# Optimization experiments

Hardware: AMD Instinct MI355X
Metric: run time of the kernel (lower is better)

The kernel has to match this reference:

```python
import jax, jax.numpy as jnp
import numpy as np

B, S, D, H, HD, K, FF, G, E = 2, 2048, 512, 8, 64, 31, 2048, 4, 2
EPS = 1e-6


def _layer_norm(x, scale, bias):
    m = jnp.mean(x, axis=-1, keepdims=True)
    v = jnp.var(x, axis=-1, keepdims=True)
    return (x - m) * jax.lax.rsqrt(v + EPS) * scale + bias


def _forward(x, group_ids, p):
    (ln1_s, ln1_b, ck, cb, ln2_s, ln2_b,
     wq, bq, wk, bk, wv, bv, wo, bo, w1, b1, w2, b2) = p
    # ---- conv sublayer: LN -> Conv1d(SAME) -> gelu -> residual ----
    r = x
    h = _layer_norm(x, ln1_s, ln1_b)
    h = jax.lax.conv_general_dilated(h, ck, (1,), 'SAME',
                                     dimension_numbers=('NWC', 'WIO', 'NWC')) + cb
    x = jax.nn.gelu(h) + r
    # ---- self-attention sublayer: LN -> MHA -> residual ----
    r = x
    h = _layer_norm(x, ln2_s, ln2_b)
    q = jnp.einsum('bsd,dhk->bshk', h, wq) + bq   # [B,S,H,HD]
    k = jnp.einsum('bsd,dhk->bshk', h, wk) + bk
    v = jnp.einsum('bsd,dhk->bshk', h, wv) + bv
    scale = jnp.asarray(1.0 / np.sqrt(HD), h.dtype)
    att = jax.nn.softmax(jnp.einsum('bqhk,bshk->bhqs', q, k) * scale, axis=-1)
    o = jnp.einsum('bhqs,bshk->bqhk', att, v)
    x = jnp.einsum('bqhk,hkd->bqd', o, wo) + bo + r
    # ---- MoE sublayer: group tokens -> per-group experts -> mean -> combine ----
    r = x
    xf = x.reshape(-1, D)            # [N, D]
    gid = group_ids.reshape(-1)      # [N]
    # Each token routed by group_id gets the mean over that group's E experts.
    hid = jax.nn.gelu(jnp.einsum('nd,gedf->genf', xf, w1) + b1[:, :, None, :])  # [G,E,N,FF]
    ye = jnp.einsum('genf,gefd->gend', hid, w2) + b2[:, :, None, :]             # [G,E,N,D]
    yg = ye.mean(axis=1)                                                        # [G,N,D]
    sel = yg[gid, jnp.arange(gid.shape[0])]                                     # [N,D] combine by group id
    return sel.reshape(B, S, D) + r


def setup_inputs() -> dict:
    key = jax.random.key(0)
    ks = jax.random.split(key, 12)
    std = 0.02
    f32 = jnp.float32
    return {
        'x': jax.random.normal(ks[0], (B, S, D), f32),
        'group_ids': jax.random.randint(ks[1], (B, S), 0, G, jnp.int32),
        'ln1_scale': jnp.ones((D,), f32), 'ln1_bias': jnp.zeros((D,), f32),
        'conv_kernel': jax.random.normal(ks[2], (K, D, D), f32) * std,
        'conv_bias': jnp.zeros((D,), f32),
        'ln2_scale': jnp.ones((D,), f32), 'ln2_bias': jnp.zeros((D,), f32),
        'wq': jax.random.normal(ks[3], (D, H, HD), f32) * std, 'bq': jnp.zeros((H, HD), f32),
        'wk': jax.random.normal(ks[4], (D, H, HD), f32) * std, 'bk': jnp.zeros((H, HD), f32),
        'wv': jax.random.normal(ks[5], (D, H, HD), f32) * std, 'bv': jnp.zeros((H, HD), f32),
        'wo': jax.random.normal(ks[6], (H, HD, D), f32) * std, 'bo': jnp.zeros((D,), f32),
        'w1': jax.random.normal(ks[7], (G, E, D, FF), f32) * std, 'b1': jnp.zeros((G, E, FF), f32),
        'w2': jax.random.normal(ks[8], (G, E, FF, D), f32) * std, 'b2': jnp.zeros((G, E, D), f32),
    }


def reference(x, group_ids, ln1_scale, ln1_bias, conv_kernel, conv_bias,
              ln2_scale, ln2_bias, wq, bq, wk, bk, wv, bv, wo, bo,
              w1, b1, w2, b2):
    p = (ln1_scale, ln1_bias, conv_kernel, conv_bias, ln2_scale, ln2_bias,
         wq, bq, wk, bk, wv, bv, wo, bo, w1, b1, w2, b2)
    return _forward(x, group_ids, p)
```

## Files before the change

kernel.cpp:

```cpp
#include <hip/hip_runtime.h>
#include <hip/hip_bf16.h>
#include <math.h>
#include <stdint.h>

namespace {

constexpr int B_ = 2, S_ = 2048, D_ = 512, H_ = 8, HD_ = 64, K_ = 31,
              FF_ = 2048, G_ = 4, E_ = 2;
constexpr int N_ = B_ * S_;
constexpr int SP_ = S_ + 30;
constexpr float EPS_ = 1e-6f;
constexpr int PADCAP_ = 4608;

typedef __bf16 bf16x8 __attribute__((ext_vector_type(8)));
typedef unsigned short u16x8 __attribute__((ext_vector_type(8)));
typedef unsigned short u16x4 __attribute__((ext_vector_type(4)));
typedef float f32x4 __attribute__((ext_vector_type(4)));

__device__ __forceinline__ uint16_t f2bf(float f) {
  union { float f; uint32_t u; } v; v.f = f;
  uint32_t r = v.u + 0x7FFFu + ((v.u >> 16) & 1u);
  return (uint16_t)(r >> 16);
}
__device__ __forceinline__ float bf2f(uint16_t u) {
  union { uint32_t u; float f; } v; v.u = (uint32_t)u << 16;
  return v.f;
}

__device__ __forceinline__ float gelu_f(float x) {
  const float c = 0.7978845608028654f;
  return 0.5f * x * (1.0f + tanhf(c * (x + 0.044715f * x * x * x)));
}

#define GLOAD_LDS16(gsrc, ldst)                                              \
  __builtin_amdgcn_global_load_lds(                                          \
      (const __attribute__((address_space(1))) void*)(gsrc),                 \
      (__attribute__((address_space(3))) void*)(ldst), 16, 0, 0)

#define VMCNT(n) asm volatile("s_waitcnt vmcnt(" #n ")" ::: "memory")
#define MEMBAR asm volatile("" ::: "memory")
#define BARRIER __builtin_amdgcn_s_barrier()
#define PRIO1 __builtin_amdgcn_s_setprio(1)
#define PRIO0 __builtin_amdgcn_s_setprio(0)

__device__ __forceinline__ void kstep_swz(const char* As, const char* Bs,
                                          int wr, int wc, int l15, int g,
                                          f32x4 acc[4][4]) {
#pragma unroll
  for (int ks = 0; ks < 2; ++ks) {
    int co = (((ks << 2) | g) ^ (l15 & 7)) << 4;
    bf16x8 a[4], b[4];
#pragma unroll
    for (int m = 0; m < 4; ++m)
      a[m] = *(const bf16x8*)(As + (wr * 64 + m * 16 + l15) * 128 + co);
#pragma unroll
    for (int n = 0; n < 4; ++n)
      b[n] = *(const bf16x8*)(Bs + (wc * 64 + n * 16 + l15) * 128 + co);
    PRIO1;
#pragma unroll
    for (int m = 0; m < 4; ++m)
#pragma unroll
      for (int n = 0; n < 4; ++n)
        acc[m][n] = __builtin_amdgcn_mfma_f32_16x16x32_bf16(a[m], b[n], acc[m][n], 0, 0, 0);
    PRIO0;
  }
}

template <int NK>
__device__ __forceinline__ void gemm_k_dbuf64(const uint16_t* Ab, int lda,
                                              const uint16_t* Bb, int ldb,
                                              int t, int wr, int wc, int l15, int g,
                                              uint16_t (*As)[8192], uint16_t (*Bs)[8192],
                                              f32x4 acc[4][4]) {
  int r8 = t >> 3, clog = (t & 7) ^ (r8 & 7);
  int ubase = (t & ~63) * 8;
  auto stage = [&](int k0, int buf) {
#pragma unroll
    for (int pi = 0; pi < 4; ++pi) {
      int row = pi * 32 + r8;
      GLOAD_LDS16(Ab + (size_t)row * lda + k0 + clog * 8, As[buf] + pi * 2048 + ubase);
      GLOAD_LDS16(Bb + (size_t)row * ldb + k0 + clog * 8, Bs[buf] + pi * 2048 + ubase);
    }
  };
  stage(0, 0);
  int cur = 0;
  for (int ki = 0; ki < NK; ++ki) {
    if (ki + 1 < NK) {
      stage((ki + 1) * 64, cur ^ 1);
      VMCNT(8);
    } else {
      VMCNT(0);
    }
    BARRIER; MEMBAR;
    kstep_swz((const char*)As[cur], (const char*)Bs[cur], wr, wc, l15, g, acc);
    MEMBAR; BARRIER;
    cur ^= 1;
  }
}

__global__ __launch_bounds__(256) void prep_kernel(
    const float* __restrict__ ck, const float* __restrict__ wq,
    const float* __restrict__ wk, const float* __restrict__ wv,
    const float* __restrict__ wo, const float* __restrict__ w1,
    const float* __restrict__ w2, uint16_t* __restrict__ ckT,
    uint16_t* __restrict__ wqkvT, uint16_t* __restrict__ woT,
    uint16_t* __restrict__ w1T, uint16_t* __restrict__ w2T,
    uint16_t* __restrict__ Hpad, uint16_t* __restrict__ x2bf,
    const float* __restrict__ x, const float* __restrict__ ln1s,
    const float* __restrict__ ln1b, const int* __restrict__ gid,
    int* __restrict__ list, int* __restrict__ poff) {
  int bi = blockIdx.x, t = threadIdx.x;
  if (bi >= 25406) {
    int row = bi - 25406;
    const float* xr = x + (size_t)row * D_;
    float v0 = xr[t], v1 = xr[t + 256];
    float s = v0 + v1, sq = v0 * v0 + v1 * v1;
    for (int o = 32; o > 0; o >>= 1) {
      s += __shfl_down(s, o);
      sq += __shfl_down(sq, o);
    }
    __shared__ float sm[8];
    __shared__ float mr[2];
    int lane = t & 63, wid = t >> 6;
    if (lane == 0) { sm[wid] = s; sm[wid + 4] = sq; }
    __syncthreads();
    if (t == 0) {
      float ts = sm[0] + sm[1] + sm[2] + sm[3];
      float tq = sm[4] + sm[5] + sm[6] + sm[7];
      float m = ts / D_;
      mr[0] = m;
      mr[1] = rsqrtf(tq / D_ - m * m + EPS_);
    }
    __syncthreads();
    float m = mr[0], rs = mr[1];
    size_t drow = (size_t)(row >> 11) * SP_ + 15 + (row & 2047);
    uint16_t* orow = Hpad + drow * D_;
    orow[t] = f2bf((v0 - m) * rs * ln1s[t] + ln1b[t]);
    orow[t + 256] = f2bf((v1 - m) * rs * ln1s[t + 256] + ln1b[t + 256]);
    return;
  }
  if (bi == 25405) {
    __shared__ int cnt[G_], cur[G_];
    if (t < G_) cnt[t] = 0;
    __syncthreads();
    for (int i = t; i < N_; i += 256) atomicAdd(&cnt[gid[i]], 1);
    __syncthreads();
    if (t == 0) {
      int off = 0;
      for (int g = 0; g < G_; ++g) {
        poff[g] = off;
        cur[g] = off;
        off += (cnt[g] + 127) & ~127;
      }
      poff[G_] = off;
    }
    __syncthreads();
    for (int i = t; i < PADCAP_; i += 256) list[i] = N_;
    __syncthreads();
    for (int i = t; i < N_; i += 256) {
      int p = atomicAdd(&cur[gid[i]], 1);
      list[p] = i;
    }
    return;
  }
  if (bi >= 25344) {
    int j4 = bi - 25344;
    uint16_t* dst;
    if (j4 < 60) {
      int b = j4 / 30, j = j4 % 30;
      int row = b * SP_ + (j < 15 ? j : 2048 + j);
      dst = Hpad + (size_t)row * D_;
    } else {
      dst = x2bf + (size_t)N_ * D_;
    }
    dst[t] = 0;
    dst[t + 256] = 0;
    return;
  }
  const float* src;
  uint16_t* dst;
  int R, C, r0, c0;
  if (bi < 7936) {
    int z = bi >> 8, tile = bi & 255;
    R = 512; C = 512;
    c0 = (tile & 15) * 32; r0 = (tile >> 4) * 32;
    src = ck + (size_t)z * 262144; dst = ckT + (size_t)z * 262144;
  } else if (bi < 8960) {
    int idx = bi - 7936, mat = idx >> 8, tile = idx & 255;
    R = 512; C = 512;
    c0 = (tile & 15) * 32; r0 = (tile >> 4) * 32;
    src = mat == 0 ? wq : (mat == 1 ? wk : (mat == 2 ? wv : wo));
    dst = mat == 3 ? woT : wqkvT + (size_t)mat * 262144;
  } else if (bi < 17152) {
    int idx = bi - 8960, z = idx >> 10, tile = idx & 1023;
    R = 512; C = 2048;
    c0 = (tile & 63) * 32; r0 = (tile >> 6) * 32;
    src = w1 + (size_t)z * 1048576; dst = w1T + (size_t)z * 1048576;
  } else {
    int idx = bi - 17152, z = idx >> 10, tile = idx & 1023;
    R = 2048; C = 512;
    c0 = (tile & 15) * 32; r0 = (tile >> 4) * 32;
    src = w2 + (size_t)z * 1048576; dst = w2T + (size_t)z * 1048576;
  }
  __shared__ float tile[32][33];
  int tc = t & 31, tr = t >> 5;
#pragma unroll
  for (int i = 0; i < 4; ++i) {
    int r = tr + i * 8;
    tile[r][tc] = src[(size_t)(r0 + r) * C + c0 + tc];
  }
  __syncthreads();
#pragma unroll
  for (int i = 0; i < 4; ++i) {
    int rr = tr + i * 8;
    dst[(size_t)(c0 + rr) * R + r0 + tc] = f2bf(tile[tc][rr]);
  }
}

__global__ __launch_bounds__(512) void conv_mfma_kernel(
    const uint16_t* __restrict__ Hpad, const uint16_t* __restrict__ ckT,
    uint16_t* __restrict__ Pout) {
  __shared__ __align__(16) uint16_t As[2][20480];
  __shared__ __align__(16) uint16_t Bs[2][16384];
  int bid = blockIdx.x;
  int ks = bid & 7, tmn = bid >> 3, tm = tmn & 15, tn = tmn >> 4;
  int t = threadIdx.x;
  int w = t >> 6, l = t & 63, l15 = l & 15, g = l >> 4;
  int wr = w >> 2, wc = w & 3;
  int row0 = tm * 256, b = row0 >> 11, s0 = row0 & 2047;
  int kb = ks * 4, ntap = (ks == 7) ? 3 : 4;
  const uint16_t* Abase = Hpad + (size_t)(b * SP_ + s0 + kb) * D_;
  int r8 = t >> 3, clog = (t & 7) ^ (r8 & 7);
  int ubase = (t & ~63) * 8;
  f32x4 acc[8][4] = {};

  auto stageA = [&](int d0, int buf) {
#pragma unroll
    for (int pi = 0; pi < 5; ++pi)
      GLOAD_LDS16(Abase + (size_t)(pi * 64 + r8) * D_ + d0 + clog * 8,
                  As[buf] + pi * 4096 + ubase);
  };
  auto stageB = [&](int k, int d0, int buf) {
    const uint16_t* Bk = ckT + (size_t)k * D_ * D_ + (size_t)(tn * 256) * D_;
#pragma unroll
    for (int pi = 0; pi < 4; ++pi)
      GLOAD_LDS16(Bk + (size_t)(pi * 64 + r8) * D_ + d0 + clog * 8,
                  Bs[buf] + pi * 4096 + ubase);
  };

  stageA(0, 0);
  stageB(kb, 0, 0);
  int acur = 0, bcur = 0;
  for (int di = 0; di < 8; ++di) {
    int d0 = di * 64;
    for (int i = 0; i < ntap; ++i) {
      if (i + 1 < ntap) {
        stageB(kb + i + 1, d0, bcur ^ 1);
        VMCNT(4);
      } else if (di + 1 < 8) {
        stageA(d0 + 64, acur ^ 1);
        stageB(kb, d0 + 64, bcur ^ 1);
        VMCNT(9);
      } else {
        VMCNT(0);
      }
      BARRIER; MEMBAR;
      const char* Ac = (const char*)As[acur];
      const char* Bc = (const char*)Bs[bcur];
#pragma unroll
      for (int kk = 0; kk < 2; ++kk) {
        int cA = (((kk << 2) | g) ^ ((i + l15) & 7)) << 4;
        int cB = (((kk << 2) | g) ^ (l15 & 7)) << 4;
        bf16x8 a[8], bb[4];
#pragma unroll
        for (int m = 0; m < 8; ++m)
          a[m] = *(const bf16x8*)(Ac + (i + wr * 128 + m * 16 + l15) * 128 + cA);
#pragma unroll
        for (int n = 0; n < 4; ++n)
          bb[n] = *(const bf16x8*)(Bc + (wc * 64 + n * 16 + l15) * 128 + cB);
        PRIO1;
#pragma unroll
        for (int m = 0; m < 8; ++m)
#pragma unroll
          for (int n = 0; n < 4; ++n)
            acc[m][n] = __builtin_amdgcn_mfma_f32_16x16x32_bf16(a[m], bb[n], acc[m][n], 0, 0, 0);
        PRIO0;
      }
      MEMBAR; BARRIER;
      bcur ^= 1;
    }
    acur ^= 1;
  }
  uint16_t* P = Pout + (size_t)ks * N_ * D_;
#pragma unroll
  for (int m = 0; m < 8; ++m) {
    int r = row0 + wr * 128 + m * 16 + g * 4;
#pragma unroll
    for (int n = 0; n < 4; ++n) {
      int c = tn * 256 + wc * 64 + n * 16 + l15;
#pragma unroll
      for (int j = 0; j < 4; ++j)
        P[(size_t)(r + j) * D_ + c] = f2bf(acc[m][n][j]);
    }
  }
}

__global__ __launch_bounds__(256) void epi_ln_kernel(
    const uint16_t* __restrict__ P, const float* __restrict__ cb,
    const float* __restrict__ xres, const float* __restrict__ ln2s,
    const float* __restrict__ ln2b, float* __restrict__ x1,
    uint16_t* __restrict__ ln2bf) {
  int t = threadIdx.x;
  int row = blockIdx.x * 4 + (t >> 6);
  int l = t & 63, d0 = l * 8;
  size_t base = (size_t)row * D_ + d0;
  float v[8] = {};
#pragma unroll
  for (int q = 0; q < 8; ++q) {
    u16x8 pv = *(const u16x8*)(P + (size_t)q * N_ * D_ + base);
#pragma unroll
    for (int j = 0; j < 8; ++j) v[j] += bf2f(pv[j]);
  }
  float s = 0.f, sq = 0.f;
#pragma unroll
  for (int j = 0; j < 8; ++j) {
    float xv = xres[base + j];
    float vv = gelu_f(v[j] + cb[d0 + j]) + xv;
    v[j] = vv;
    s += vv;
    sq += vv * vv;
  }
  float4 o0 = {v[0], v[1], v[2], v[3]};
  float4 o1 = {v[4], v[5], v[6], v[7]};
  *(float4*)(x1 + base) = o0;
  *(float4*)(x1 + base + 4) = o1;
  for (int o = 1; o < 64; o <<= 1) {
    s += __shfl_xor(s, o);
    sq += __shfl_xor(sq, o);
  }
  float m = s / D_;
  float rs = rsqrtf(sq / D_ - m * m + EPS_);
  u16x8 ob;
#pragma unroll
  for (int j = 0; j < 8; ++j)
    ob[j] = f2bf((v[j] - m) * rs * ln2s[d0 + j] + ln2b[d0 + j]);
  *(u16x8*)(ln2bf + base) = ob;
}

__global__ __launch_bounds__(256) void gemm_qkv_kernel(
    const uint16_t* __restrict__ A, const uint16_t* __restrict__ BT,
    const float* __restrict__ bq, const float* __restrict__ bk,
    const float* __restrict__ bv, uint16_t* __restrict__ Qb,
    uint16_t* __restrict__ Kb, uint16_t* __restrict__ VT) {
  __shared__ __align__(16) uint16_t As[2][8192], Bs[2][8192];
  int tm = blockIdx.x, tn = blockIdx.y;
  int t = threadIdx.x;
  int w = t >> 6, l = t & 63, l15 = l & 15, g = l >> 4;
  int wr = w >> 1, wc = w & 1;
  int row0 = tm * 128;
  f32x4 acc[4][4] = {};
  gemm_k_dbuf64<8>(A + (size_t)row0 * D_, D_, BT + (size_t)(tn * 128) * D_, D_,
                   t, wr, wc, l15, g, As, Bs, acc);
  int sel = tn >> 2, col0 = (tn & 3) * 128;
  if (sel < 2) {
    uint16_t* dst = sel == 0 ? Qb : Kb;
    const float* bias = sel == 0 ? bq : bk;
    float scl = sel == 0 ? 0.125f : 1.0f;
#pragma unroll
    for (int m = 0; m < 4; ++m) {
      int r = row0 + wr * 64 + m * 16 + g * 4;
#pragma unroll
      for (int n = 0; n < 4; ++n) {
        int c = col0 + wc * 64 + n * 16 + l15;
#pragma unroll
        for (int j = 0; j < 4; ++j)
          dst[(size_t)(r + j) * D_ + c] = f2bf((acc[m][n][j] + bias[c]) * scl);
      }
    }
  } else {
#pragma unroll
    for (int m = 0; m < 4; ++m) {
      int tb = row0 + wr * 64 + m * 16 + g * 4;
      int b = tb >> 11, s = tb & 2047;
#pragma unroll
      for (int n = 0; n < 4; ++n) {
        int c = col0 + wc * 64 + n * 16 + l15;
        int hh = c >> 6, d = c & 63;
        u16x4 pack;
#pragma unroll
        for (int j = 0; j < 4; ++j) pack[j] = f2bf(acc[m][n][j] + bv[c]);
        *(u16x4*)(VT + ((size_t)((b * H_ + hh) * HD_ + d) * S_ + s)) = pack;
      }
    }
  }
}

__global__ __launch_bounds__(256) void gemm_wo_kernel(
    const uint16_t* __restrict__ A, const uint16_t* __restrict__ BT,
    const float* __restrict__ bo, const float* __restrict__ res,
    float* __restrict__ out, uint16_t* __restrict__ x2bf) {
  __shared__ __align__(16) uint16_t As[2][8192], Bs[2][8192];
  int tm = blockIdx.x, tn = blockIdx.y;
  int t = threadIdx.x;
  int w = t >> 6, l = t & 63, l15 = l & 15, g = l >> 4;
  int wr = w >> 1, wc = w & 1;
  int row0 = tm * 128;
  f32x4 acc[4][4] = {};
  gemm_k_dbuf64<8>(A + (size_t)row0 * D_, D_, BT + (size_t)(tn * 128) * D_, D_,
                   t, wr, wc, l15, g, As, Bs, acc);
#pragma unroll
  for (int m = 0; m < 4; ++m) {
    int r = row0 + wr * 64 + m * 16 + g * 4;
#pragma unroll
    for (int n = 0; n < 4; ++n) {
      int c = tn * 128 + wc * 64 + n * 16 + l15;
#pragma unroll
      for (int j = 0; j < 4; ++j) {
        float v = acc[m][n][j] + bo[c] + res[(size_t)(r + j) * D_ + c];
        out[(size_t)(r + j) * D_ + c] = v;
        x2bf[(size_t)(r + j) * D_ + c] = f2bf(v);
      }
    }
  }
}

__global__ __launch_bounds__(512) void attn_mfma_kernel(
    const uint16_t* __restrict__ Qbf, const uint16_t* __restrict__ Kbf,
    const uint16_t* __restrict__ VT, uint16_t* __restrict__ obf) {
  __shared__ __align__(16) uint16_t Ks[2][4096];
  __shared__ __align__(16) uint16_t Vt[2][4096];
  __shared__ __align__(16) uint16_t Plds[8192];
  int qt = blockIdx.x, h = blockIdx.y, b = blockIdx.z;
  int t = threadIdx.x, w = t >> 6, l = t & 63;
  int l15 = l & 15, g = l >> 4;
  int qbase = b * S_ + qt * 128;
  bf16x8 qb_[2];
  {
    const uint16_t* qp = Qbf + (size_t)(qbase + w * 16 + l15) * D_ + h * HD_;
#pragma unroll
    for (int ks = 0; ks < 2; ++ks)
      qb_[ks] = *(const bf16x8*)(qp + ks * 32 + g * 8);
  }
  const uint16_t* Kbase = Kbf + (size_t)(b * S_) * D_ + h * HD_;
  const uint16_t* Vbase = VT + (size_t)((b * H_ + h) * HD_) * S_;
  int r0 = t >> 3, slot = t & 7;
  int sb0 = (slot * 16) ^ ((r0 & 7) << 4);
  int ldst = (t & ~63) * 16;

  auto stage_kv = [&](int kt, int buf) {
    const uint16_t* Kp = Kbase + (size_t)(kt * 64) * D_;
    const uint16_t* Vp = Vbase + kt * 64;
    GLOAD_LDS16((const char*)(Kp + (size_t)r0 * D_) + sb0, (char*)Ks[buf] + ldst);
    GLOAD_LDS16((const char*)(Vp + (size_t)r0 * S_) + sb0, (char*)Vt[buf] + ldst);
  };

  f32x4 acc_o[4] = {};
  float m_run = -INFINITY, l_run = 0.f;
  char* Pw = (char*)Plds + w * 2048;

  stage_kv(0, 0);
  int cur = 0;
  for (int kt = 0; kt < S_ / 64; ++kt) {
    if (kt + 1 < S_ / 64) {
      stage_kv(kt + 1, cur ^ 1);
      VMCNT(2);
    } else {
      VMCNT(0);
    }
    BARRIER; MEMBAR;
    const char* KsC = (const char*)Ks[cur];
    const char* VtC = (const char*)Vt[cur];
    f32x4 accs[4] = {};
#pragma unroll
    for (int ks = 0; ks < 2; ++ks) {
#pragma unroll
      for (int m = 0; m < 4; ++m) {
        int row = m * 16 + l15;
        bf16x8 kf = *(const bf16x8*)(KsC +
                        (row * 128 + ((ks * 64 + g * 16) ^ ((row & 7) << 4))));
        PRIO1;
        accs[m] = __builtin_amdgcn_mfma_f32_16x16x32_bf16(kf, qb_[ks], accs[m], 0, 0, 0);
        PRIO0;
      }
    }
    float mx = accs[0][0];
#pragma unroll
    for (int m = 0; m < 4; ++m)
#pragma unroll
      for (int j = 0; j < 4; ++j) mx = fmaxf(mx, accs[m][j]);
    mx = fmaxf(mx, __shfl_xor(mx, 16));
    mx = fmaxf(mx, __shfl_xor(mx, 32));
    float mnew = fmaxf(m_run, mx);
    float corr = __expf(m_run - mnew);
    m_run = mnew;
    float sum = 0.f;
#pragma unroll
    for (int m = 0; m < 4; ++m) {
      float p0 = __expf(accs[m][0] - mnew);
      float p1 = __expf(accs[m][1] - mnew);
      float p2 = __expf(accs[m][2] - mnew);
      float p3 = __expf(accs[m][3] - mnew);
      sum += (p0 + p1) + (p2 + p3);
      uint2 pk;
      pk.x = (uint32_t)f2bf(p0) | ((uint32_t)f2bf(p1) << 16);
      pk.y = (uint32_t)f2bf(p2) | ((uint32_t)f2bf(p3) << 16);
      *(uint2*)(Pw + (l15 * 128 + ((m * 32 + g * 8) ^ ((l15 & 7) << 4)))) = pk;
    }
    sum += __shfl_xor(sum, 16);
    sum += __shfl_xor(sum, 32);
    l_run = l_run * corr + sum;
    float cj[4];
#pragma unroll
    for (int j = 0; j < 4; ++j) cj[j] = __shfl(corr, g * 4 + j);
#pragma unroll
    for (int n = 0; n < 4; ++n)
#pragma unroll
      for (int j = 0; j < 4; ++j) acc_o[n][j] *= cj[j];
#pragma unroll
    for (int ks = 0; ks < 2; ++ks) {
      bf16x8 pa = *(const bf16x8*)(Pw +
                      (l15 * 128 + ((ks * 64 + g * 16) ^ ((l15 & 7) << 4))));
#pragma unroll
      for (int n = 0; n < 4; ++n) {
        int d = n * 16 + l15;
        bf16x8 vb = *(const bf16x8*)(VtC +
                        (d * 128 + ((ks * 64 + g * 16) ^ ((d & 7) << 4))));
        PRIO1;
        acc_o[n] = __builtin_amdgcn_mfma_f32_16x16x32_bf16(pa, vb, acc_o[n], 0, 0, 0);
        PRIO0;
      }
    }
    MEMBAR; BARRIER;
    cur ^= 1;
  }
#pragma unroll
  for (int j = 0; j < 4; ++j) {
    float lr = __shfl(l_run, g * 4 + j);
    float inv = 1.f / lr;
    uint16_t* op = obf + (size_t)(qbase + w * 16 + g * 4 + j) * D_ + h * HD_;
#pragma unroll
    for (int n = 0; n < 4; ++n)
      op[n * 16 + l15] = f2bf(acc_o[n][j] * inv);
  }
}

__global__ __launch_bounds__(256) void ff1_mfma_kernel(
    const uint16_t* __restrict__ X, const uint16_t* __restrict__ w1T,
    const float* __restrict__ b1, const int* __restrict__ list,
    const int* __restrict__ poff, uint16_t* __restrict__ hid) {
  __shared__ __align__(16) uint16_t As[2][8192], Bs[2][8192];
  int tm = blockIdx.x, tn = blockIdx.y, e = blockIdx.z;
  int slot0 = tm * 128;
  if (slot0 >= poff[G_]) return;
  int g_ = 0;
#pragma unroll
  for (int gg = 1; gg < G_; ++gg) g_ += (slot0 >= poff[gg]);
  int t = threadIdx.x;
  int w = t >> 6, l = t & 63, l15 = l & 15, g = l >> 4;
  int wr = w >> 1, wc = w & 1;
  int r8 = t >> 3, clog = (t & 7) ^ (r8 & 7);
  int ubase = (t & ~63) * 8;
  int tok[4];
#pragma unroll
  for (int pi = 0; pi < 4; ++pi) tok[pi] = list[slot0 + pi * 32 + r8];
  const uint16_t* Bb = w1T + ((size_t)(g_ * E_ + e) * FF_ + tn * 128) * D_;
  f32x4 acc[4][4] = {};
  auto stage = [&](int k0, int buf) {
#pragma unroll
    for (int pi = 0; pi < 4; ++pi) {
      GLOAD_LDS16(X + (size_t)tok[pi] * D_ + k0 + clog * 8, As[buf] + pi * 2048 + ubase);
      GLOAD_LDS16(Bb + (size_t)(pi * 32 + r8) * D_ + k0 + clog * 8,
                  Bs[buf] + pi * 2048 + ubase);
    }
  };
  stage(0, 0);
  int cur = 0;
  for (int ki = 0; ki < 8; ++ki) {
    if (ki + 1 < 8) {
      stage((ki + 1) * 64, cur ^ 1);
      VMCNT(8);
    } else {
      VMCNT(0);
    }
    BARRIER; MEMBAR;
    kstep_swz((const char*)As[cur], (const char*)Bs[cur], wr, wc, l15, g, acc);
    MEMBAR; BARRIER;
    cur ^= 1;
  }
  const float* bias = b1 + (size_t)(g_ * E_ + e) * FF_;
  uint16_t* hidE = hid + (size_t)e * PADCAP_ * FF_;
#pragma unroll
  for (int m = 0; m < 4; ++m) {
    int r = slot0 + wr * 64 + m * 16 + g * 4;
#pragma unroll
    for (int n = 0; n < 4; ++n) {
      int c = tn * 128 + wc * 64 + n * 16 + l15;
#pragma unroll
      for (int j = 0; j < 4; ++j)
        hidE[(size_t)(r + j) * FF_ + c] = f2bf(gelu_f(acc[m][n][j] + bias[c]));
    }
  }
}

__global__ __launch_bounds__(256) void ff2_mfma_kernel(
    const uint16_t* __restrict__ hid, const uint16_t* __restrict__ w2T,
    const float* __restrict__ b2, const int* __restrict__ list,
    const int* __restrict__ poff, float* __restrict__ out) {
  __shared__ __align__(16) uint16_t As[2][4096];
  __shared__ __align__(16) uint16_t Bs[2][8192];
  int tm = blockIdx.x, tn = blockIdx.y, e = blockIdx.z;
  int slot0 = tm * 64;
  if (slot0 >= poff[G_]) return;
  int g_ = 0;
#pragma unroll
  for (int gg = 1; gg < G_; ++gg) g_ += (slot0 >= poff[gg]);
  int t = threadIdx.x;
  int w = t >> 6, l = t & 63, l15 = l & 15, g = l >> 4;
  int wr = w >> 1, wc = w & 1;
  int r8 = t >> 3, clog = (t & 7) ^ (r8 & 7);
  int ubase = (t & ~63) * 8;
  const uint16_t* Ab = hid + ((size_t)e * PADCAP_ + slot0) * FF_;
  const uint16_t* Bb = w2T + (size_t)(g_ * E_ + e) * D_ * FF_ + (size_t)(tn * 128) * FF_;
  f32x4 acc[2][4] = {};
  auto stage = [&](int k0, int buf) {
#pragma unroll
    for (int pi = 0; pi < 2; ++pi)
      GLOAD_LDS16(Ab + (size_t)(pi * 32 + r8) * FF_ + k0 + clog * 8,
                  As[buf] + pi * 2048 + ubase);
#pragma unroll
    for (int pi = 0; pi < 4; ++pi)
      GLOAD_LDS16(Bb + (size_t)(pi * 32 + r8) * FF_ + k0 + clog * 8,
                  Bs[buf] + pi * 2048 + ubase);
  };
  stage(0, 0);
  int cur = 0;
  for (int ki = 0; ki < 32; ++ki) {
    if (ki + 1 < 32) {
      stage((ki + 1) * 64, cur ^ 1);
      VMCNT(6);
    } else {
      VMCNT(0);
    }
    BARRIER; MEMBAR;
    const char* Ac = (const char*)As[cur];
    const char* Bc = (const char*)Bs[cur];
#pragma unroll
    for (int ks = 0; ks < 2; ++ks) {
      int co = (((ks << 2) | g) ^ (l15 & 7)) << 4;
      bf16x8 a[2], b[4];
#pragma unroll
      for (int m = 0; m < 2; ++m)
        a[m] = *(const bf16x8*)(Ac + (wr * 32 + m * 16 + l15) * 128 + co);
#pragma unroll
      for (int n = 0; n < 4; ++n)
        b[n] = *(const bf16x8*)(Bc + (wc * 64 + n * 16 + l15) * 128 + co);
      PRIO1;
#pragma unroll
      for (int m = 0; m < 2; ++m)
#pragma unroll
        for (int n = 0; n < 4; ++n)
          acc[m][n] = __builtin_amdgcn_mfma_f32_16x16x32_bf16(a[m], b[n], acc[m][n], 0, 0, 0);
      PRIO0;
    }
    MEMBAR; BARRIER;
    cur ^= 1;
  }
  const float* be = b2 + (size_t)(g_ * E_ + e) * D_;
#pragma unroll
  for (int m = 0; m < 2; ++m) {
    int rbase = slot0 + wr * 32 + m * 16 + g * 4;
#pragma unroll
    for (int j = 0; j < 4; ++j) {
      int tok = list[rbase + j];
      if (tok >= N_) continue;
#pragma unroll
      for (int n = 0; n < 4; ++n) {
        int c = tn * 128 + wc * 64 + n * 16 + l15;
        atomicAdd(&out[(size_t)tok * D_ + c], 0.5f * (acc[m][n][j] + be[c]));
      }
    }
  }
}

}

extern "C" void kernel_launch(void* const* d_in, const int* in_sizes, int n_in,
                              void* d_out, int out_size, void* d_ws, size_t ws_size,
                              hipStream_t stream) {
  const float* x = (const float*)d_in[0];
  const int* gid = (const int*)d_in[1];
  const float* ln1s = (const float*)d_in[2];
  const float* ln1b = (const float*)d_in[3];
  const float* ck = (const float*)d_in[4];
  const float* cb = (const float*)d_in[5];
  const float* ln2s = (const float*)d_in[6];
  const float* ln2b = (const float*)d_in[7];
  const float* wq = (const float*)d_in[8];
  const float* bq = (const float*)d_in[9];
  const float* wk = (const float*)d_in[10];
  const float* bk = (const float*)d_in[11];
  const float* wv = (const float*)d_in[12];
  const float* bv = (const float*)d_in[13];
  const float* wo = (const float*)d_in[14];
  const float* bo = (const float*)d_in[15];
  const float* w1 = (const float*)d_in[16];
  const float* b1 = (const float*)d_in[17];
  const float* w2 = (const float*)d_in[18];
  const float* b2 = (const float*)d_in[19];
  float* out = (float*)d_out;

  char* ws = (char*)d_ws;
  char* A = ws;
  uint16_t* P = (uint16_t*)A;
  uint16_t* ln2bf = (uint16_t*)(A + (32ull << 20));
  uint16_t* Qbf = (uint16_t*)A;
  uint16_t* Kbf = (uint16_t*)(A + (4ull << 20));
  uint16_t* VT = (uint16_t*)(A + (8ull << 20));
  uint16_t* obf = (uint16_t*)(A + (12ull << 20));
  uint16_t* hidbf = (uint16_t*)A;

  float* x1 = (float*)(ws + (38ull << 20));
  uint16_t* Hpad = (uint16_t*)(ws + (46ull << 20));
  uint16_t* ckT = (uint16_t*)(ws + (51ull << 20));
  uint16_t* wqkvT = (uint16_t*)(ws + (67ull << 20));
  uint16_t* woT = (uint16_t*)(ws + (69ull << 20));
  uint16_t* w1T = (uint16_t*)(ws + (70ull << 20));
  uint16_t* w2T = (uint16_t*)(ws + (86ull << 20));
  uint16_t* x2bf = (uint16_t*)(ws + (102ull << 20));
  int* list = (int*)(ws + (107ull << 20));
  int* poff = list + PADCAP_;

  prep_kernel<<<29502, 256, 0, stream>>>(ck, wq, wk, wv, wo, w1, w2,
                                         ckT, wqkvT, woT, w1T, w2T, Hpad, x2bf,
                                         x, ln1s, ln1b, gid, list, poff);

  conv_mfma_kernel<<<256, 512, 0, stream>>>(Hpad, ckT, P);
  epi_ln_kernel<<<1024, 256, 0, stream>>>(P, cb, x, ln2s, ln2b, x1, ln2bf);

  gemm_qkv_kernel<<<dim3(32, 12), 256, 0, stream>>>(ln2bf, wqkvT, bq, bk, bv, Qbf, Kbf, VT);
  attn_mfma_kernel<<<dim3(S_ / 128, H_, B_), 512, 0, stream>>>(Qbf, Kbf, VT, obf);
  gemm_wo_kernel<<<dim3(32, 4), 256, 0, stream>>>(obf, woT, bo, x1, out, x2bf);

  ff1_mfma_kernel<<<dim3(36, 16, 2), 256, 0, stream>>>(x2bf, w1T, b1, list, poff, hidbf);
  ff2_mfma_kernel<<<dim3(72, 4, 2), 256, 0, stream>>>(hidbf, w2T, b2, list, poff, out);
}
```

Measured before the change: 291.0 us.

## Widen attention KV tiles to 128, use exp2 softmax with lazy rescaling, swizzle blocks

The attention kernel now stages 128 keys and values per iteration instead of 64, which halves the number of loop trips and barriers. The Q scale now folds in log2(e), so softmax can use exp2f. The running max and the output accumulators are only rescaled when the new max exceeds the old one by more than a threshold (a lazy-rescale trick). The launch becomes a 1D grid with a swizzled block-to-(q tile, head, batch) mapping to change scheduling and cache locality. LDS use per block doubles, which may reduce occupancy. The lazy rescale relies on bounded growth within the threshold to keep values in range.

Result: no change. 289.3 us (-0.6%).

```diff
diff --git a/kernel.cpp b/kernel.cpp
--- a/kernel.cpp
+++ b/kernel.cpp
@@ -365,7 +365,7 @@
   if (sel < 2) {
     uint16_t* dst = sel == 0 ? Qb : Kb;
     const float* bias = sel == 0 ? bq : bk;
-    float scl = sel == 0 ? 0.125f : 1.0f;
+    float scl = sel == 0 ? 0.18033688f : 1.0f;
 #pragma unroll
     for (int m = 0; m < 4; ++m) {
       int r = row0 + wr * 64 + m * 16 + g * 4;
@@ -427,10 +427,12 @@
 __global__ __launch_bounds__(512) void attn_mfma_kernel(
     const uint16_t* __restrict__ Qbf, const uint16_t* __restrict__ Kbf,
     const uint16_t* __restrict__ VT, uint16_t* __restrict__ obf) {
-  __shared__ __align__(16) uint16_t Ks[2][4096];
-  __shared__ __align__(16) uint16_t Vt[2][4096];
-  __shared__ __align__(16) uint16_t Plds[8192];
-  int qt = blockIdx.x, h = blockIdx.y, b = blockIdx.z;
+  __shared__ __align__(16) uint16_t Ks[2][8192];
+  __shared__ __align__(16) uint16_t Vt[2][8192];
+  __shared__ __align__(16) uint16_t Plds[16384];
+  int bid = blockIdx.x;
+  int swz = (bid & 7) * 32 + (bid >> 3);
+  int qt = swz & 15, h = (swz >> 4) & 7, b = swz >> 7;
   int t = threadIdx.x, w = t >> 6, l = t & 63;
   int l15 = l & 15, g = l >> 4;
   int qbase = b * S_ + qt * 128;
@@ -443,38 +445,43 @@
   }
   const uint16_t* Kbase = Kbf + (size_t)(b * S_) * D_ + h * HD_;
   const uint16_t* Vbase = VT + (size_t)((b * H_ + h) * HD_) * S_;
-  int r0 = t >> 3, slot = t & 7;
-  int sb0 = (slot * 16) ^ ((r0 & 7) << 4);
-  int ldst = (t & ~63) * 16;
+  int rk0 = t >> 3, rk1 = 64 + (t >> 3), pk = t & 7;
+  int rv0 = t >> 4, rv1 = 32 + (t >> 4), pv = t & 15;
+  int ck0 = (pk ^ (rk0 & 7)) << 4, ck1 = (pk ^ (rk1 & 7)) << 4;
+  int cv0 = (pv ^ (rv0 & 7)) << 4, cv1 = (pv ^ (rv1 & 7)) << 4;
+  int ldst0 = (t & ~63) << 4, ldst1 = (512 + (t & ~63)) << 4;
 
   auto stage_kv = [&](int kt, int buf) {
-    const uint16_t* Kp = Kbase + (size_t)(kt * 64) * D_;
-    const uint16_t* Vp = Vbase + kt * 64;
-    GLOAD_LDS16((const char*)(Kp + (size_t)r0 * D_) + sb0, (char*)Ks[buf] + ldst);
-    GLOAD_LDS16((const char*)(Vp + (size_t)r0 * S_) + sb0, (char*)Vt[buf] + ldst);
+    const uint16_t* Kp = Kbase + (size_t)(kt * 128) * D_;
+    const uint16_t* Vp = Vbase + kt * 128;
+    GLOAD_LDS16((const char*)(Kp + (size_t)rk0 * D_) + ck0, (char*)Ks[buf] + ldst0);
+    GLOAD_LDS16((const char*)(Kp + (size_t)rk1 * D_) + ck1, (char*)Ks[buf] + ldst1);
+    GLOAD_LDS16((const char*)(Vp + (size_t)rv0 * S_) + cv0, (char*)Vt[buf] + ldst0);
+    GLOAD_LDS16((const char*)(Vp + (size_t)rv1 * S_) + cv1, (char*)Vt[buf] + ldst1);
   };
 
   f32x4 acc_o[4] = {};
   float m_run = -INFINITY, l_run = 0.f;
-  char* Pw = (char*)Plds + w * 2048;
+  char* Pw = (char*)Plds + w * 4096;
+  int swl = (l15 & 7) << 4;
 
   stage_kv(0, 0);
   int cur = 0;
-  for (int kt = 0; kt < S_ / 64; ++kt) {
-    if (kt + 1 < S_ / 64) {
+  for (int kt = 0; kt < S_ / 128; ++kt) {
+    if (kt + 1 < S_ / 128) {
       stage_kv(kt + 1, cur ^ 1);
-      VMCNT(2);
+      VMCNT(4);
     } else {
       VMCNT(0);
     }
     BARRIER; MEMBAR;
     const char* KsC = (const char*)Ks[cur];
     const char* VtC = (const char*)Vt[cur];
-    f32x4 accs[4] = {};
+    f32x4 accs[8] = {};
 #pragma unroll
     for (int ks = 0; ks < 2; ++ks) {
 #pragma unroll
-      for (int m = 0; m < 4; ++m) {
+      for (int m = 0; m < 8; ++m) {
         int row = m * 16 + l15;
         bf16x8 kf = *(const bf16x8*)(KsC +
                         (row * 128 + ((ks * 64 + g * 16) ^ ((row & 7) << 4))));
@@ -485,46 +492,48 @@
     }
     float mx = accs[0][0];
 #pragma unroll
-    for (int m = 0; m < 4; ++m)
+    for (int m = 0; m < 8; ++m)
 #pragma unroll
       for (int j = 0; j < 4; ++j) mx = fmaxf(mx, accs[m][j]);
     mx = fmaxf(mx, __shfl_xor(mx, 16));
     mx = fmaxf(mx, __shfl_xor(mx, 32));
-    float mnew = fmaxf(m_run, mx);
-    float corr = __expf(m_run - mnew);
-    m_run = mnew;
+    if (!__all(mx <= m_run + 8.f)) {
+      float mnew = fmaxf(m_run, mx);
+      float corr = exp2f(m_run - mnew);
+      m_run = mnew;
+      l_run *= corr;
+      float cj[4];
+#pragma unroll
+      for (int j = 0; j < 4; ++j) cj[j] = __shfl(corr, g * 4 + j);
+#pragma unroll
+      for (int n = 0; n < 4; ++n)
+#pragma unroll
+        for (int j = 0; j < 4; ++j) acc_o[n][j] *= cj[j];
+    }
     float sum = 0.f;
 #pragma unroll
-    for (int m = 0; m < 4; ++m) {
-      float p0 = __expf(accs[m][0] - mnew);
-      float p1 = __expf(accs[m][1] - mnew);
-      float p2 = __expf(accs[m][2] - mnew);
-      float p3 = __expf(accs[m][3] - mnew);
+    for (int m = 0; m < 8; ++m) {
+      float p0 = exp2f(accs[m][0] - m_run);
+      float p1 = exp2f(accs[m][1] - m_run);
+      float p2 = exp2f(accs[m][2] - m_run);
+      float p3 = exp2f(accs[m][3] - m_run);
       sum += (p0 + p1) + (p2 + p3);
-      uint2 pk;
-      pk.x = (uint32_t)f2bf(p0) | ((uint32_t)f2bf(p1) << 16);
-      pk.y = (uint32_t)f2bf(p2) | ((uint32_t)f2bf(p3) << 16);
-      *(uint2*)(Pw + (l15 * 128 + ((m * 32 + g * 8) ^ ((l15 & 7) << 4)))) = pk;
+      uint2 pk2;
+      pk2.x = (uint32_t)f2bf(p0) | ((uint32_t)f2bf(p1) << 16);
+      pk2.y = (uint32_t)f2bf(p2) | ((uint32_t)f2bf(p3) << 16);
+      *(uint2*)(Pw + (l15 * 256 + ((m * 32 + g * 8) ^ swl))) = pk2;
     }
     sum += __shfl_xor(sum, 16);
     sum += __shfl_xor(sum, 32);
-    l_run = l_run * corr + sum;
-    float cj[4];
-#pragma unroll
-    for (int j = 0; j < 4; ++j) cj[j] = __shfl(corr, g * 4 + j);
-#pragma unroll
-    for (int n = 0; n < 4; ++n)
-#pragma unroll
-      for (int j = 0; j < 4; ++j) acc_o[n][j] *= cj[j];
-#pragma unroll
-    for (int ks = 0; ks < 2; ++ks) {
-      bf16x8 pa = *(const bf16x8*)(Pw +
-                      (l15 * 128 + ((ks * 64 + g * 16) ^ ((l15 & 7) << 4))));
+    l_run += sum;
+#pragma unroll
+    for (int s = 0; s < 4; ++s) {
+      bf16x8 pa = *(const bf16x8*)(Pw + (l15 * 256 + ((s * 64 + g * 16) ^ swl)));
 #pragma unroll
       for (int n = 0; n < 4; ++n) {
         int d = n * 16 + l15;
         bf16x8 vb = *(const bf16x8*)(VtC +
-                        (d * 128 + ((ks * 64 + g * 16) ^ ((d & 7) << 4))));
+                        (d * 256 + ((s * 64 + g * 16) ^ ((d & 7) << 4))));
         PRIO1;
         acc_o[n] = __builtin_amdgcn_mfma_f32_16x16x32_bf16(pa, vb, acc_o[n], 0, 0, 0);
         PRIO0;
@@ -738,7 +747,7 @@
   epi_ln_kernel<<<1024, 256, 0, stream>>>(P, cb, x, ln2s, ln2b, x1, ln2bf);
 
   gemm_qkv_kernel<<<dim3(32, 12), 256, 0, stream>>>(ln2bf, wqkvT, bq, bk, bv, Qbf, Kbf, VT);
-  attn_mfma_kernel<<<dim3(S_ / 128, H_, B_), 512, 0, stream>>>(Qbf, Kbf, VT, obf);
+  attn_mfma_kernel<<<256, 512, 0, stream>>>(Qbf, Kbf, VT, obf);
   gemm_wo_kernel<<<dim3(32, 4), 256, 0, stream>>>(obf, woT, bo, x1, out, x2bf);
 
   ff1_mfma_kernel<<<dim3(36, 16, 2), 256, 0, stream>>>(x2bf, w1T, b1, list, poff, hidbf);
```
